# Optimization experiments

Measured on AMD Instinct MI355X. Metric: run time of the kernel, lower is better.

Reference implementation:

```python
import jax, jax.numpy as jnp
import numpy as np

B, D, DEPTH, C = 131072, 64, 10, 16
N_INNER = 2 ** DEPTH - 1   # 1023 inner nodes, heap (BFS) order
N_LEAF = 2 ** DEPTH        # 1024 leaves


def setup_inputs() -> dict:
    key = jax.random.key(0)
    k1, k2, k3, k4, k5 = jax.random.split(key, 5)
    X = jax.random.normal(k1, (B, D), dtype=jnp.float32)
    W = jax.random.normal(k2, (N_INNER, D), dtype=jnp.float32) * (1.0 / np.sqrt(D))
    b = jax.random.normal(k3, (N_INNER,), dtype=jnp.float32) * (1.0 / np.sqrt(D))
    beta = jax.random.normal(k4, (N_INNER,), dtype=jnp.float32)
    leaf_params = jax.random.normal(k5, (N_LEAF, C), dtype=jnp.float32)
    return {"X": X, "W": W, "b": b, "beta": beta, "leaf_params": leaf_params}


def reference(X, W, b, beta, leaf_params):
    """Soft decision tree forward.

    Each inner node n computes p_n = sigmoid(beta_n * (x @ w_n + b_n)).
    Path prob multiplies (1-p) going left, p going right; leaves emit
    softmax(leaf_params). Returns the mixture prediction
    sum_l path_prob_l * Q_l  -> [B, C].
    """
    n_inner = W.shape[0]
    depth = int(np.log2(n_inner + 1))
    bsz = X.shape[0]

    # All inner-node gates in one GEMM: [B, N_inner]
    z = X @ W.T + b
    p = jax.nn.sigmoid(beta * z)

    # Level-by-level BFS traversal; children order [left, right] per parent
    # matches the DFS leaf order of the original recursion.
    path = jnp.ones((bsz, 1), dtype=X.dtype)
    start = 0
    for d in range(depth):
        n = 2 ** d
        pd = p[:, start:start + n]                      # [B, 2^d]
        path = jnp.stack([path * (1.0 - pd), path * pd], axis=-1).reshape(bsz, 2 * n)
        start += n

    Q = jax.nn.softmax(leaf_params, axis=-1)            # [L, C]
    out = path @ Q                                       # [B, C] mixture over leaves
    return out
```

## Files before the change

### kernel.cpp

```cpp
#include <hip/hip_runtime.h>
#include <hip/hip_bf16.h>

typedef unsigned int u32;
typedef unsigned short u16;
typedef __attribute__((ext_vector_type(4))) short bf16x4;
typedef __attribute__((ext_vector_type(8))) short bf16x8;
typedef __attribute__((ext_vector_type(4))) float f32x4;
typedef __attribute__((ext_vector_type(4))) u32 u32x4;

#define MFMA(a,b,c) __builtin_amdgcn_mfma_f32_16x16x32_bf16((a),(b),(c),0,0,0)

static constexpr int NCH = 17;

static constexpr size_t WS_WFRAG = 0;
static constexpr size_t WS_QFRAG = 278528;
static constexpr size_t WS_EBTAB = 344064;
static constexpr size_t WS_NEED  = 353024;

__device__ __forceinline__ u16 f2bf(float f){
  u32 u = __float_as_uint(f);
  return (u16)((u + 0x7fffu + ((u >> 16) & 1u)) >> 16);
}
__device__ __forceinline__ float bf2f(u16 h){ return __uint_as_float(((u32)h) << 16); }

__device__ __forceinline__ int nodemap(int ch, int n){
  if (ch == 0) return (n < 15) ? n : -1;
  if (n >= 63) return -1;
  int v = n + 1;
  int L = 31 - __clz(v);
  return ((1 << (L + 4)) - 1) + ((ch - 1) << L) + (v - (1 << L));
}

__global__ void sdt_prep(const float* __restrict__ W, const float* __restrict__ b,
                         const float* __restrict__ beta, const float* __restrict__ LP,
                         char* __restrict__ ws)
{
  const int bid = blockIdx.x, t = threadIdx.x;
  u16* wfrag = (u16*)(ws + WS_WFRAG);
  u16* qfrag = (u16*)(ws + WS_QFRAG);
  float2* eb = (float2*)(ws + WS_EBTAB);

  if (bid < 34){
    int id = bid*256 + t;
    if (id < 17*4*2*64){
      int lane = id & 63, kt = (id >> 6) & 1, ct = (id >> 7) & 3, ch = id >> 9;
      int n = ct*16 + (lane & 15);
      int g = nodemap(ch, n);
      int k0 = kt*32 + ((lane >> 4) << 3);
      size_t basH = ((((size_t)ch*4 + ct)*2 + kt)*2 + 0)*512 + (size_t)lane*8;
      size_t basL = basH + 512;
      #pragma unroll
      for (int j = 0; j < 8; ++j){
        float v = (g >= 0) ? W[(size_t)g*64 + k0 + j] : 0.0f;
        u16 h = f2bf(v);
        wfrag[basH + j] = h;
        wfrag[basL + j] = f2bf(v - bf2f(h));
      }
    }
  } else if (bid < 42){
    int id = (bid - 34)*256 + t;
    int lane = id & 63, kt = (id >> 6) & 1, s = id >> 7;
    int c = lane & 15;
    size_t basH = (((size_t)s*2 + kt)*2 + 0)*512 + (size_t)lane*8;
    size_t basL = basH + 512;
    #pragma unroll
    for (int j = 0; j < 8; ++j){
      int leaf = s*64 + kt*32 + ((lane >> 4) << 3) + j;
      const float* row = LP + (size_t)leaf*16;
      float m = row[0];
      #pragma unroll
      for (int cc = 1; cc < 16; ++cc) m = fmaxf(m, row[cc]);
      float ssum = 0.f;
      #pragma unroll
      for (int cc = 0; cc < 16; ++cc) ssum += __expf(row[cc] - m);
      float q = __expf(row[c] - m) / ssum;
      u16 h = f2bf(q);
      qfrag[basH + j] = h;
      qfrag[basL + j] = f2bf(q - bf2f(h));
    }
  } else {
    int id = (bid - 42)*256 + t;
    if (id < 17*64){
      int n = id & 63, ch = id >> 6;
      int g = nodemap(ch, n);
      float be = (g >= 0) ? beta[g] : 0.0f;
      float bb = (g >= 0) ? b[g]    : 0.0f;
      eb[id] = make_float2(-be, -be * bb);
    }
  }
}

__global__ __launch_bounds__(256, 3) void sdt_main(
    const float* __restrict__ X, const char* __restrict__ ws,
    float* __restrict__ out)
{
  __shared__ float sP[4][16*67];
  __shared__ float sPath[4][16*17];
  __shared__ char  sLp[4][4096];

  const int tid  = threadIdx.x;
  const int w    = tid >> 6;
  const int lane = tid & 63;
  const int bid  = blockIdx.x;

  const u16*    wfrag = (const u16*)(ws + WS_WFRAG);
  const u16*    qfrag = (const u16*)(ws + WS_QFRAG);
  const float2* ebTab = (const float2*)(ws + WS_EBTAB);

  char* sX = (char*)sLp;
  {
    const float4* Xg = (const float4*)X + (size_t)bid * 1024;
    #pragma unroll
    for (int i = 0; i < 4; ++i){
      int f = tid + i*256;
      float4 v = Xg[f];
      int row = f >> 4;
      int byteo = row*128 + (f & 15)*8;
      int swz = (row & 7) << 4;
      u16 h0 = f2bf(v.x), h1 = f2bf(v.y), h2 = f2bf(v.z), h3 = f2bf(v.w);
      bf16x4 hv = {(short)h0, (short)h1, (short)h2, (short)h3};
      bf16x4 lv = {(short)f2bf(v.x - bf2f(h0)), (short)f2bf(v.y - bf2f(h1)),
                   (short)f2bf(v.z - bf2f(h2)), (short)f2bf(v.w - bf2f(h3))};
      *(bf16x4*)(sX + (byteo ^ swz)) = hv;
      *(bf16x4*)(sX + 8192 + (byteo ^ swz)) = lv;
    }
  }
  __syncthreads();

  const int mA   = lane & 15;
  const int kofs = (lane >> 4) * 16;
  const int swzA = (mA & 7) << 4;
  const int rowb = (w*16 + mA) * 128;
  const bf16x8 aH0 = *(const bf16x8*)(sX + ((rowb + kofs     ) ^ swzA));
  const bf16x8 aH1 = *(const bf16x8*)(sX + ((rowb + 64 + kofs) ^ swzA));
  const bf16x8 aL0 = *(const bf16x8*)(sX + 8192 + ((rowb + kofs     ) ^ swzA));
  const bf16x8 aL1 = *(const bf16x8*)(sX + 8192 + ((rowb + 64 + kofs) ^ swzA));
  __syncthreads();

  f32x4 accO = {0.f, 0.f, 0.f, 0.f};
  const int mrow = lane >> 2;
  const int q4   = lane & 3;
  float* Pw    = sP[w];
  float* pathw = sPath[w];
  u16*   lpW   = (u16*)sLp[w];

  for (int ch = 0; ch < NCH; ++ch){
    const int s = (ch >= 1) ? (ch - 1) : 0;
    const u16* qb = qfrag + (size_t)s * 2048;
    const bf16x8 qH0 = *(const bf16x8*)(qb +    0 + lane*8);
    const bf16x8 qL0 = *(const bf16x8*)(qb +  512 + lane*8);
    const bf16x8 qH1 = *(const bf16x8*)(qb + 1024 + lane*8);
    const bf16x8 qL1 = *(const bf16x8*)(qb + 1536 + lane*8);

    const int ncts = (ch == 0) ? 1 : 4;
    const u16* wb = wfrag + (size_t)ch * 8192;
    for (int ct = 0; ct < ncts; ++ct){
      const u16* wc = wb + ct*2048;
      const bf16x8 wH0 = *(const bf16x8*)(wc +    0 + lane*8);
      const bf16x8 wL0 = *(const bf16x8*)(wc +  512 + lane*8);
      const bf16x8 wH1 = *(const bf16x8*)(wc + 1024 + lane*8);
      const bf16x8 wL1 = *(const bf16x8*)(wc + 1536 + lane*8);
      f32x4 az = {0.f, 0.f, 0.f, 0.f};
      az = MFMA(aH0, wH0, az);
      az = MFMA(aH1, wH1, az);
      az = MFMA(aH0, wL0, az);
      az = MFMA(aH1, wL1, az);
      az = MFMA(aL0, wH0, az);
      az = MFMA(aL1, wH1, az);
      const int n = ct*16 + (lane & 15);
      const float2 eb = ebTab[ch*64 + n];
      #pragma unroll
      for (int r = 0; r < 4; ++r){
        const int m = (lane >> 4)*4 + r;
        const float u = __expf(fmaf(az[r], eb.x, eb.y));
        Pw[m*67 + n] = __builtin_amdgcn_rcpf(1.0f + u);
      }
    }

    if (ch == 0){
      #pragma unroll
      for (int u = 0; u < 4; ++u){
        const int t = q4*4 + u;
        const float* Pr = &Pw[mrow*67];
        float p0 = Pr[0], p1 = Pr[1 + (t>>3)], p2 = Pr[3 + (t>>2)], p3 = Pr[7 + (t>>1)];
        float f0 = (t & 8) ? p0 : 1.f - p0;
        float f1 = (t & 4) ? p1 : 1.f - p1;
        float f2 = (t & 2) ? p2 : 1.f - p2;
        float f3 = (t & 1) ? p3 : 1.f - p3;
        pathw[mrow*17 + t] = f0*f1*f2*f3;
      }
    } else {
      const float pf = pathw[mrow*17 + s];
      const float* Pr = &Pw[mrow*67];
      const float pA = Pr[0];
      const float pB = Pr[1 + (q4 >> 1)];
      const float pC = Pr[3 + q4];
      const float lpre = pf * ((q4 & 2) ? pA : 1.f - pA) * ((q4 & 1) ? pB : 1.f - pB);
      float a2[2], a3[4], a4[8], a5[16];
      a2[0] = lpre * (1.f - pC); a2[1] = lpre * pC;
      #pragma unroll
      for (int i = 0; i < 2; ++i){
        float p = Pr[7 + 2*q4 + i];
        a3[2*i] = a2[i]*(1.f - p); a3[2*i+1] = a2[i]*p;
      }
      #pragma unroll
      for (int i = 0; i < 4; ++i){
        float p = Pr[15 + 4*q4 + i];
        a4[2*i] = a3[i]*(1.f - p); a4[2*i+1] = a3[i]*p;
      }
      #pragma unroll
      for (int i = 0; i < 8; ++i){
        float p = Pr[31 + 8*q4 + i];
        a5[2*i] = a4[i]*(1.f - p); a5[2*i+1] = a4[i]*p;
      }
      u32 hiw[8], low[8];
      #pragma unroll
      for (int i = 0; i < 8; ++i){
        u32 u0 = __float_as_uint(a5[2*i]);
        u32 u1 = __float_as_uint(a5[2*i+1]);
        hiw[i] = __builtin_amdgcn_perm(u1, u0, 0x07060302u);
        float l0 = a5[2*i]   - __uint_as_float(u0 & 0xffff0000u);
        float l1 = a5[2*i+1] - __uint_as_float(u1 & 0xffff0000u);
        low[i] = __builtin_amdgcn_perm(__float_as_uint(l1), __float_as_uint(l0), 0x07060302u);
      }
      {
        char* dh = (char*)lpW + (q4 >> 1)*1024 + (((q4 & 1)*2)*16 + mrow)*16;
        *(u32x4*)(dh       ) = u32x4{hiw[0], hiw[1], hiw[2], hiw[3]};
        *(u32x4*)(dh + 256 ) = u32x4{hiw[4], hiw[5], hiw[6], hiw[7]};
        *(u32x4*)(dh + 2048) = u32x4{low[0], low[1], low[2], low[3]};
        *(u32x4*)(dh + 2304) = u32x4{low[4], low[5], low[6], low[7]};
      }
      const char* lb = (const char*)lpW + lane*16;
      const bf16x8 pH0 = *(const bf16x8*)(lb       );
      const bf16x8 pH1 = *(const bf16x8*)(lb + 1024);
      const bf16x8 pL0 = *(const bf16x8*)(lb + 2048);
      const bf16x8 pL1 = *(const bf16x8*)(lb + 3072);
      accO = MFMA(pH0, qH0, accO);
      accO = MFMA(pH1, qH1, accO);
      accO = MFMA(pL0, qH0, accO);
      accO = MFMA(pL1, qH1, accO);
      accO = MFMA(pH0, qL0, accO);
      accO = MFMA(pH1, qL1, accO);
    }
  }

  const size_t ob = ((size_t)bid*64 + w*16) * 16 + (lane & 15);
  #pragma unroll
  for (int r = 0; r < 4; ++r){
    const int m = (lane >> 4)*4 + r;
    out[ob + (size_t)m*16] = accO[r];
  }
}

extern "C" void kernel_launch(void* const* d_in, const int* in_sizes, int n_in,
                              void* d_out, int out_size, void* d_ws, size_t ws_size,
                              hipStream_t stream)
{
  const float* X    = (const float*)d_in[0];
  const float* W    = (const float*)d_in[1];
  const float* b    = (const float*)d_in[2];
  const float* beta = (const float*)d_in[3];
  const float* LP   = (const float*)d_in[4];
  float* out = (float*)d_out;
  char*  ws  = (char*)d_ws;

  if (ws_size < WS_NEED) return;

  sdt_prep<<<47, 256, 0, stream>>>(W, b, beta, LP, ws);
  sdt_main<<<2048, 256, 0, stream>>>(X, ws, out);
}
```

Before: 121.7 us.

## Swizzle gate LDS layout, keep path prefix in registers, use exp2 and raise occupancy

The padded gate buffer (stride 67) becomes a 256-byte-row layout with an XOR swizzle, and all per-lane read addresses are precomputed before the chunk loop. The depth-4 path prefixes stay in registers and are fetched across lanes with ds_bpermute, so the sPath shared array goes away. The sigmoid folds log2(e) into the precomputed beta/bias table and uses exp2 directly. Launch bounds rise from 3 to 4 blocks per SM, which cuts LDS use and instruction count but risks register pressure or spills.

```diff
diff --git a/kernel.cpp b/kernel.cpp
--- a/kernel.cpp
+++ b/kernel.cpp
@@ -39,6 +39,7 @@
   u16* wfrag = (u16*)(ws + WS_WFRAG);
   u16* qfrag = (u16*)(ws + WS_QFRAG);
   float2* eb = (float2*)(ws + WS_EBTAB);
+  const float LOG2E = 1.4426950408889634f;
 
   if (bid < 34){
     int id = bid*256 + t;
@@ -85,23 +86,25 @@
       int g = nodemap(ch, n);
       float be = (g >= 0) ? beta[g] : 0.0f;
       float bb = (g >= 0) ? b[g]    : 0.0f;
-      eb[id] = make_float2(-be, -be * bb);
+      eb[id] = make_float2(-be * LOG2E, -be * bb * LOG2E);
     }
   }
 }
 
-__global__ __launch_bounds__(256, 3) void sdt_main(
+__global__ __launch_bounds__(256, 4) void sdt_main(
     const float* __restrict__ X, const char* __restrict__ ws,
     float* __restrict__ out)
 {
-  __shared__ float sP[4][16*67];
-  __shared__ float sPath[4][16*17];
+  __shared__ float sP[4][1024];
   __shared__ char  sLp[4][4096];
 
   const int tid  = threadIdx.x;
   const int w    = tid >> 6;
   const int lane = tid & 63;
   const int bid  = blockIdx.x;
+
+  float* Pw  = sP[w];
+  u16*   lpW = (u16*)sLp[w];
 
   const u16*    wfrag = (const u16*)(ws + WS_WFRAG);
   const u16*    qfrag = (const u16*)(ws + WS_QFRAG);
@@ -140,9 +143,30 @@
   f32x4 accO = {0.f, 0.f, 0.f, 0.f};
   const int mrow = lane >> 2;
   const int q4   = lane & 3;
-  float* Pw    = sP[w];
-  float* pathw = sPath[w];
-  u16*   lpW   = (u16*)sLp[w];
+  const int nIdx = lane & 15;
+  const int grp4 = (lane >> 4) * 4;
+
+  char*     Pwr = (char*)Pw + grp4*256;
+  const int gx  = (grp4 & 4) << 4;
+  const int nb4 = nIdx*4;
+  char*     Pb  = (char*)Pw + mrow*256;
+  const int rx  = (mrow & 7) << 4;
+  auto PXp = [&](int c){ return (const float*)(Pb + ((c << 2) ^ rx)); };
+  const float* ApA = PXp(0);
+  const float* ApB = PXp(1 + (q4 >> 1));
+  const float* ApC = PXp(3 + q4);
+  const float* Ap3[2];
+  #pragma unroll
+  for (int j = 0; j < 2; ++j) Ap3[j] = PXp(7 + 2*q4 + j);
+  const float* Ap4[4];
+  #pragma unroll
+  for (int j = 0; j < 4; ++j) Ap4[j] = PXp(15 + 4*q4 + j);
+  const float* Ap5[8];
+  #pragma unroll
+  for (int j = 0; j < 8; ++j) Ap5[j] = PXp(31 + 8*q4 + j);
+
+  float pfv[4];
+  const int lbase = (lane & 60) << 2;
 
   for (int ch = 0; ch < NCH; ++ch){
     const int s = (ch >= 1) ? (ch - 1) : 0;
@@ -167,13 +191,12 @@
       az = MFMA(aH1, wL1, az);
       az = MFMA(aL0, wH0, az);
       az = MFMA(aL1, wH1, az);
-      const int n = ct*16 + (lane & 15);
-      const float2 eb = ebTab[ch*64 + n];
+      const float2 eb = ebTab[ch*64 + ct*16 + nIdx];
+      const int colx = (ct*64 + nb4) ^ gx;
       #pragma unroll
       for (int r = 0; r < 4; ++r){
-        const int m = (lane >> 4)*4 + r;
-        const float u = __expf(fmaf(az[r], eb.x, eb.y));
-        Pw[m*67 + n] = __builtin_amdgcn_rcpf(1.0f + u);
+        const float u = __builtin_amdgcn_exp2f(fmaf(az[r], eb.x, eb.y));
+        *(float*)(Pwr + r*256 + (colx ^ (r << 4))) = __builtin_amdgcn_rcpf(1.0f + u);
       }
     }
 
@@ -181,36 +204,42 @@
       #pragma unroll
       for (int u = 0; u < 4; ++u){
         const int t = q4*4 + u;
-        const float* Pr = &Pw[mrow*67];
-        float p0 = Pr[0], p1 = Pr[1 + (t>>3)], p2 = Pr[3 + (t>>2)], p3 = Pr[7 + (t>>1)];
+        float p0  = *PXp(0);
+        float p1  = *PXp(1 + (t>>3));
+        float p2  = *PXp(3 + (t>>2));
+        float p3v = *PXp(7 + (t>>1));
         float f0 = (t & 8) ? p0 : 1.f - p0;
         float f1 = (t & 4) ? p1 : 1.f - p1;
         float f2 = (t & 2) ? p2 : 1.f - p2;
-        float f3 = (t & 1) ? p3 : 1.f - p3;
-        pathw[mrow*17 + t] = f0*f1*f2*f3;
+        float f3 = (t & 1) ? p3v : 1.f - p3v;
+        pfv[u] = f0*f1*f2*f3;
       }
     } else {
-      const float pf = pathw[mrow*17 + s];
-      const float* Pr = &Pw[mrow*67];
-      const float pA = Pr[0];
-      const float pB = Pr[1 + (q4 >> 1)];
-      const float pC = Pr[3 + q4];
+      const float va   = (s & 1) ? pfv[1] : pfv[0];
+      const float vb   = (s & 1) ? pfv[3] : pfv[2];
+      const float vsel = (s & 2) ? vb : va;
+      const int   paddr = lbase | (s & 12);
+      const float pf = __uint_as_float((u32)__builtin_amdgcn_ds_bpermute(paddr, (int)__float_as_uint(vsel)));
+
+      const float pA = *ApA;
+      const float pB = *ApB;
+      const float pC = *ApC;
       const float lpre = pf * ((q4 & 2) ? pA : 1.f - pA) * ((q4 & 1) ? pB : 1.f - pB);
       float a2[2], a3[4], a4[8], a5[16];
       a2[0] = lpre * (1.f - pC); a2[1] = lpre * pC;
       #pragma unroll
       for (int i = 0; i < 2; ++i){
-        float p = Pr[7 + 2*q4 + i];
+        float p = *Ap3[i];
         a3[2*i] = a2[i]*(1.f - p); a3[2*i+1] = a2[i]*p;
       }
       #pragma unroll
       for (int i = 0; i < 4; ++i){
-        float p = Pr[15 + 4*q4 + i];
+        float p = *Ap4[i];
         a4[2*i] = a3[i]*(1.f - p); a4[2*i+1] = a3[i]*p;
       }
       #pragma unroll
       for (int i = 0; i < 8; ++i){
-        float p = Pr[31 + 8*q4 + i];
+        float p = *Ap5[i];
         a5[2*i] = a4[i]*(1.f - p); a5[2*i+1] = a4[i]*p;
       }
       u32 hiw[8], low[8];
```

New measurement: 125.0 us. 2.8% more time.

## Software-pipeline gate GEMM one chunk ahead of path mixing; fold log2e into exp

Applied to the files above, without the earlier changes.

The chunk loop is restructured so the MFMA gate products for the next subtree chunk are issued before the sigmoid, path-product and mixture work of the current chunk, using two register sets of accumulators in a ping-pong scheme. This is meant to hide MFMA and global weight-load latency behind the VALU and LDS work of the previous chunk. The prep kernel also pre-scales the beta/bias table by log2(e) so the kernel can call the native exp2 directly. The extra live accumulators raise register pressure, which could hurt occupancy under the 3-blocks launch bound.

```diff
diff --git a/kernel.cpp b/kernel.cpp
--- a/kernel.cpp
+++ b/kernel.cpp
@@ -10,7 +10,6 @@
 
 #define MFMA(a,b,c) __builtin_amdgcn_mfma_f32_16x16x32_bf16((a),(b),(c),0,0,0)
 
-static constexpr int NCH = 17;
 
 static constexpr size_t WS_WFRAG = 0;
 static constexpr size_t WS_QFRAG = 278528;
@@ -39,6 +38,7 @@
   u16* wfrag = (u16*)(ws + WS_WFRAG);
   u16* qfrag = (u16*)(ws + WS_QFRAG);
   float2* eb = (float2*)(ws + WS_EBTAB);
+  const float LOG2E = 1.4426950408889634f;
 
   if (bid < 34){
     int id = bid*256 + t;
@@ -85,7 +85,7 @@
       int g = nodemap(ch, n);
       float be = (g >= 0) ? beta[g] : 0.0f;
       float bb = (g >= 0) ? b[g]    : 0.0f;
-      eb[id] = make_float2(-be, -be * bb);
+      eb[id] = make_float2(-be * LOG2E, -be * bb * LOG2E);
     }
   }
 }
@@ -102,6 +102,10 @@
   const int w    = tid >> 6;
   const int lane = tid & 63;
   const int bid  = blockIdx.x;
+
+  float* Pw    = sP[w];
+  float* pathw = sPath[w];
+  u16*   lpW   = (u16*)sLp[w];
 
   const u16*    wfrag = (const u16*)(ws + WS_WFRAG);
   const u16*    qfrag = (const u16*)(ws + WS_QFRAG);
@@ -140,114 +144,141 @@
   f32x4 accO = {0.f, 0.f, 0.f, 0.f};
   const int mrow = lane >> 2;
   const int q4   = lane & 3;
-  float* Pw    = sP[w];
-  float* pathw = sPath[w];
-  u16*   lpW   = (u16*)sLp[w];
-
-  for (int ch = 0; ch < NCH; ++ch){
-    const int s = (ch >= 1) ? (ch - 1) : 0;
+  const int nIdx = lane & 15;
+  const int grp4 = (lane >> 4) * 4;
+
+  auto zct = [&](const u16* wc, f32x4& azo){
+    const bf16x8 wH0 = *(const bf16x8*)(wc +    0 + lane*8);
+    const bf16x8 wL0 = *(const bf16x8*)(wc +  512 + lane*8);
+    const bf16x8 wH1 = *(const bf16x8*)(wc + 1024 + lane*8);
+    const bf16x8 wL1 = *(const bf16x8*)(wc + 1536 + lane*8);
+    f32x4 a = {0.f, 0.f, 0.f, 0.f};
+    a = MFMA(aH0, wH0, a);
+    a = MFMA(aH1, wH1, a);
+    a = MFMA(aH0, wL0, a);
+    a = MFMA(aH1, wL1, a);
+    a = MFMA(aL0, wH0, a);
+    a = MFMA(aL1, wH1, a);
+    azo = a;
+  };
+  auto zchunk = [&](int ch, f32x4& z0, f32x4& z1, f32x4& z2, f32x4& z3){
+    const u16* wb = wfrag + (size_t)ch * 8192;
+    zct(wb       , z0);
+    zct(wb + 2048, z1);
+    zct(wb + 4096, z2);
+    zct(wb + 6144, z3);
+  };
+
+  auto sigstore = [&](int ch, int ct, const f32x4& az){
+    const float2 eb = ebTab[ch*64 + ct*16 + nIdx];
+    #pragma unroll
+    for (int r = 0; r < 4; ++r){
+      const int m = grp4 + r;
+      const float u = __builtin_amdgcn_exp2f(fmaf(az[r], eb.x, eb.y));
+      Pw[m*67 + ct*16 + nIdx] = __builtin_amdgcn_rcpf(1.0f + u);
+    }
+  };
+
+  auto mix = [&](int ch, const f32x4& z0, const f32x4& z1, const f32x4& z2, const f32x4& z3){
+    const int s = ch - 1;
+    sigstore(ch, 0, z0);
+    sigstore(ch, 1, z1);
+    sigstore(ch, 2, z2);
+    sigstore(ch, 3, z3);
+
     const u16* qb = qfrag + (size_t)s * 2048;
     const bf16x8 qH0 = *(const bf16x8*)(qb +    0 + lane*8);
     const bf16x8 qL0 = *(const bf16x8*)(qb +  512 + lane*8);
     const bf16x8 qH1 = *(const bf16x8*)(qb + 1024 + lane*8);
     const bf16x8 qL1 = *(const bf16x8*)(qb + 1536 + lane*8);
 
-    const int ncts = (ch == 0) ? 1 : 4;
-    const u16* wb = wfrag + (size_t)ch * 8192;
-    for (int ct = 0; ct < ncts; ++ct){
-      const u16* wc = wb + ct*2048;
-      const bf16x8 wH0 = *(const bf16x8*)(wc +    0 + lane*8);
-      const bf16x8 wL0 = *(const bf16x8*)(wc +  512 + lane*8);
-      const bf16x8 wH1 = *(const bf16x8*)(wc + 1024 + lane*8);
-      const bf16x8 wL1 = *(const bf16x8*)(wc + 1536 + lane*8);
-      f32x4 az = {0.f, 0.f, 0.f, 0.f};
-      az = MFMA(aH0, wH0, az);
-      az = MFMA(aH1, wH1, az);
-      az = MFMA(aH0, wL0, az);
-      az = MFMA(aH1, wL1, az);
-      az = MFMA(aL0, wH0, az);
-      az = MFMA(aL1, wH1, az);
-      const int n = ct*16 + (lane & 15);
-      const float2 eb = ebTab[ch*64 + n];
-      #pragma unroll
-      for (int r = 0; r < 4; ++r){
-        const int m = (lane >> 4)*4 + r;
-        const float u = __expf(fmaf(az[r], eb.x, eb.y));
-        Pw[m*67 + n] = __builtin_amdgcn_rcpf(1.0f + u);
-      }
-    }
-
-    if (ch == 0){
-      #pragma unroll
-      for (int u = 0; u < 4; ++u){
-        const int t = q4*4 + u;
-        const float* Pr = &Pw[mrow*67];
-        float p0 = Pr[0], p1 = Pr[1 + (t>>3)], p2 = Pr[3 + (t>>2)], p3 = Pr[7 + (t>>1)];
-        float f0 = (t & 8) ? p0 : 1.f - p0;
-        float f1 = (t & 4) ? p1 : 1.f - p1;
-        float f2 = (t & 2) ? p2 : 1.f - p2;
-        float f3 = (t & 1) ? p3 : 1.f - p3;
-        pathw[mrow*17 + t] = f0*f1*f2*f3;
-      }
-    } else {
-      const float pf = pathw[mrow*17 + s];
-      const float* Pr = &Pw[mrow*67];
-      const float pA = Pr[0];
-      const float pB = Pr[1 + (q4 >> 1)];
-      const float pC = Pr[3 + q4];
-      const float lpre = pf * ((q4 & 2) ? pA : 1.f - pA) * ((q4 & 1) ? pB : 1.f - pB);
-      float a2[2], a3[4], a4[8], a5[16];
-      a2[0] = lpre * (1.f - pC); a2[1] = lpre * pC;
-      #pragma unroll
-      for (int i = 0; i < 2; ++i){
-        float p = Pr[7 + 2*q4 + i];
-        a3[2*i] = a2[i]*(1.f - p); a3[2*i+1] = a2[i]*p;
-      }
-      #pragma unroll
-      for (int i = 0; i < 4; ++i){
-        float p = Pr[15 + 4*q4 + i];
-        a4[2*i] = a3[i]*(1.f - p); a4[2*i+1] = a3[i]*p;
-      }
-      #pragma unroll
-      for (int i = 0; i < 8; ++i){
-        float p = Pr[31 + 8*q4 + i];
-        a5[2*i] = a4[i]*(1.f - p); a5[2*i+1] = a4[i]*p;
-      }
-      u32 hiw[8], low[8];
-      #pragma unroll
-      for (int i = 0; i < 8; ++i){
-        u32 u0 = __float_as_uint(a5[2*i]);
-        u32 u1 = __float_as_uint(a5[2*i+1]);
-        hiw[i] = __builtin_amdgcn_perm(u1, u0, 0x07060302u);
-        float l0 = a5[2*i]   - __uint_as_float(u0 & 0xffff0000u);
-        float l1 = a5[2*i+1] - __uint_as_float(u1 & 0xffff0000u);
-        low[i] = __builtin_amdgcn_perm(__float_as_uint(l1), __float_as_uint(l0), 0x07060302u);
-      }
-      {
-        char* dh = (char*)lpW + (q4 >> 1)*1024 + (((q4 & 1)*2)*16 + mrow)*16;
-        *(u32x4*)(dh       ) = u32x4{hiw[0], hiw[1], hiw[2], hiw[3]};
-        *(u32x4*)(dh + 256 ) = u32x4{hiw[4], hiw[5], hiw[6], hiw[7]};
-        *(u32x4*)(dh + 2048) = u32x4{low[0], low[1], low[2], low[3]};
-        *(u32x4*)(dh + 2304) = u32x4{low[4], low[5], low[6], low[7]};
-      }
-      const char* lb = (const char*)lpW + lane*16;
-      const bf16x8 pH0 = *(const bf16x8*)(lb       );
-      const bf16x8 pH1 = *(const bf16x8*)(lb + 1024);
-      const bf16x8 pL0 = *(const bf16x8*)(lb + 2048);
-      const bf16x8 pL1 = *(const bf16x8*)(lb + 3072);
-      accO = MFMA(pH0, qH0, accO);
-      accO = MFMA(pH1, qH1, accO);
-      accO = MFMA(pL0, qH0, accO);
-      accO = MFMA(pL1, qH1, accO);
-      accO = MFMA(pH0, qL0, accO);
-      accO = MFMA(pH1, qL1, accO);
-    }
-  }
+    const float pf = pathw[mrow*17 + s];
+    const float* Pr = &Pw[mrow*67];
+    const float pA = Pr[0];
+    const float pB = Pr[1 + (q4 >> 1)];
+    const float pC = Pr[3 + q4];
+    const float lpre = pf * ((q4 & 2) ? pA : 1.f - pA) * ((q4 & 1) ? pB : 1.f - pB);
+    float a2[2], a3[4], a4[8], a5[16];
+    a2[0] = lpre * (1.f - pC); a2[1] = lpre * pC;
+    #pragma unroll
+    for (int i = 0; i < 2; ++i){
+      float p = Pr[7 + 2*q4 + i];
+      a3[2*i] = a2[i]*(1.f - p); a3[2*i+1] = a2[i]*p;
+    }
+    #pragma unroll
+    for (int i = 0; i < 4; ++i){
+      float p = Pr[15 + 4*q4 + i];
+      a4[2*i] = a3[i]*(1.f - p); a4[2*i+1] = a3[i]*p;
+    }
+    #pragma unroll
+    for (int i = 0; i < 8; ++i){
+      float p = Pr[31 + 8*q4 + i];
+      a5[2*i] = a4[i]*(1.f - p); a5[2*i+1] = a4[i]*p;
+    }
+    u32 hiw[8], low[8];
+    #pragma unroll
+    for (int i = 0; i < 8; ++i){
+      u32 u0 = __float_as_uint(a5[2*i]);
+      u32 u1 = __float_as_uint(a5[2*i+1]);
+      hiw[i] = __builtin_amdgcn_perm(u1, u0, 0x07060302u);
+      float l0 = a5[2*i]   - __uint_as_float(u0 & 0xffff0000u);
+      float l1 = a5[2*i+1] - __uint_as_float(u1 & 0xffff0000u);
+      low[i] = __builtin_amdgcn_perm(__float_as_uint(l1), __float_as_uint(l0), 0x07060302u);
+    }
+    {
+      char* dh = (char*)lpW + (q4 >> 1)*1024 + (((q4 & 1)*2)*16 + mrow)*16;
+      *(u32x4*)(dh       ) = u32x4{hiw[0], hiw[1], hiw[2], hiw[3]};
+      *(u32x4*)(dh + 256 ) = u32x4{hiw[4], hiw[5], hiw[6], hiw[7]};
+      *(u32x4*)(dh + 2048) = u32x4{low[0], low[1], low[2], low[3]};
+      *(u32x4*)(dh + 2304) = u32x4{low[4], low[5], low[6], low[7]};
+    }
+    const char* lb = (const char*)lpW + lane*16;
+    const bf16x8 pH0 = *(const bf16x8*)(lb       );
+    const bf16x8 pH1 = *(const bf16x8*)(lb + 1024);
+    const bf16x8 pL0 = *(const bf16x8*)(lb + 2048);
+    const bf16x8 pL1 = *(const bf16x8*)(lb + 3072);
+    accO = MFMA(pH0, qH0, accO);
+    accO = MFMA(pH1, qH1, accO);
+    accO = MFMA(pL0, qH0, accO);
+    accO = MFMA(pL1, qH1, accO);
+    accO = MFMA(pH0, qL0, accO);
+    accO = MFMA(pH1, qL1, accO);
+  };
+
+  f32x4 azA0, azA1, azA2, azA3, azB0, azB1, azB2, azB3;
+  {
+    f32x4 azP;
+    zct(wfrag, azP);
+    zchunk(1, azA0, azA1, azA2, azA3);
+    sigstore(0, 0, azP);
+    const float* Pr = &Pw[mrow*67];
+    #pragma unroll
+    for (int u = 0; u < 4; ++u){
+      const int t = q4*4 + u;
+      float p0 = Pr[0], p1 = Pr[1 + (t>>3)], p2 = Pr[3 + (t>>2)], p3 = Pr[7 + (t>>1)];
+      float f0 = (t & 8) ? p0 : 1.f - p0;
+      float f1 = (t & 4) ? p1 : 1.f - p1;
+      float f2 = (t & 2) ? p2 : 1.f - p2;
+      float f3 = (t & 1) ? p3 : 1.f - p3;
+      pathw[mrow*17 + t] = f0*f1*f2*f3;
+    }
+  }
+
+  for (int sp = 0; sp < 7; ++sp){
+    const int chA = 2*sp + 1, chB = 2*sp + 2;
+    zchunk(chB, azB0, azB1, azB2, azB3);
+    mix(chA, azA0, azA1, azA2, azA3);
+    zchunk(chB + 1, azA0, azA1, azA2, azA3);
+    mix(chB, azB0, azB1, azB2, azB3);
+  }
+  zchunk(16, azB0, azB1, azB2, azB3);
+  mix(15, azA0, azA1, azA2, azA3);
+  mix(16, azB0, azB1, azB2, azB3);
 
   const size_t ob = ((size_t)bid*64 + w*16) * 16 + (lane & 15);
   #pragma unroll
   for (int r = 0; r < 4; ++r){
-    const int m = (lane >> 4)*4 + r;
+    const int m = grp4 + r;
     out[ob + (size_t)m*16] = accO[r];
   }
 }
```

Measured after the change: 136.1 us. 1.12x slower.
